# Optimization experiments

Measured on AMD Instinct MI355X. Metric: run time of the kernel, lower is better.

The kernel has to match this reference:

```python
import jax, jax.numpy as jnp
import numpy as np

B, C, H, W = 2, 128, 64, 64
D_STATE, D_CONV, EXPAND = 16, 4, 2
D_INNER = EXPAND * C
DT_RANK = (C + 15) // 16  # ceil(d_model/16) = 8


def layernorm(x, w, b):
    # WithBias_LayerNorm over last (channel) dim, unbiased=False variance
    mu = jnp.mean(x, axis=-1, keepdims=True)
    var = jnp.mean((x - mu) ** 2, axis=-1, keepdims=True)
    return (x - mu) / jnp.sqrt(var + 1e-5) * w + b


def causal_conv1d_silu(x, w, b):
    # x: (b, d, l); w: (d, k) depthwise; causal pad k-1 on left, then SiLU
    k = w.shape[1]
    out = jax.lax.conv_general_dilated(
        x, w[:, None, :], window_strides=(1,), padding=[(k - 1, 0)],
        dimension_numbers=('NCH', 'OIH', 'NCH'), feature_group_count=w.shape[0])
    return jax.nn.silu(out + b[:, None])


def selective_scan(dA, dBu, Cm):
    # dA, dBu: (b, d, l, n); Cm: (b, n, l) -> y: (b, d, l)
    dA_t = jnp.moveaxis(dA, 2, 0)    # (l, b, d, n)
    dBu_t = jnp.moveaxis(dBu, 2, 0)  # (l, b, d, n)
    C_t = jnp.moveaxis(Cm, 2, 0)     # (l, b, n)

    def step(h, inp):
        a, bu, c = inp
        h = a * h + bu
        y = jnp.einsum('bdn,bn->bd', h, c)
        return h, y

    h0 = jnp.zeros(dA.shape[:2] + (dA.shape[3],), dA.dtype)
    _, ys = jax.lax.scan(step, h0, (dA_t, dBu_t, C_t))
    return jnp.moveaxis(ys, 0, 2)  # (b, d, l)


def mamba_branch(x3, W_in, W_z, conv_w, conv_b, W_x, W_dt, b_dt, A, D, W_out):
    # x3: (b, l, d_model) normalized input
    x = jnp.einsum('bld,ed->bel', x3, W_in)  # (b, d_inner, l)
    z = jnp.einsum('bld,ed->bel', x3, W_z)
    x = causal_conv1d_silu(x, conv_w, conv_b)
    xdbl = jnp.einsum('bdl,ed->bel', x, W_x)  # (b, dt_rank+2n, l)
    dt_low = xdbl[:, :DT_RANK]
    Bm = xdbl[:, DT_RANK:DT_RANK + D_STATE]
    Cm = xdbl[:, DT_RANK + D_STATE:]
    delta = jax.nn.softplus(jnp.einsum('brl,dr->bdl', dt_low, W_dt) + b_dt[:, None])
    dA = jnp.exp(delta[:, :, :, None] * A[None, :, None, :])           # (b,d,l,n)
    dBu = jnp.einsum('bdl,bnl->bdln', delta * x, Bm)                    # (b,d,l,n)
    y = selective_scan(dA, dBu, Cm)
    y = y + D[:, None] * x
    y = y * jax.nn.silu(z)
    return jnp.einsum('bdl,od->blo', y, W_out)  # (b, l, d_model)


def setup_inputs() -> dict:
    key = jax.random.key(0)
    ks = jax.random.split(key, 24)
    rn = lambda k, shp, s: jax.random.normal(k, shp, dtype=jnp.float32) * s
    inp = {}
    inp['pan'] = rn(ks[0], (B, C, H, W), 1.0)
    inp['ms'] = rn(ks[1], (B, C, H, W), 1.0)
    inp['norm_w_pan'] = jnp.ones((C,), jnp.float32)
    inp['norm_b_pan'] = jnp.zeros((C,), jnp.float32)
    inp['norm_w_ms'] = jnp.ones((C,), jnp.float32)
    inp['norm_b_ms'] = jnp.zeros((C,), jnp.float32)
    inp['W_in_pan'] = rn(ks[2], (D_INNER, C), C ** -0.5)
    inp['W_in_ms'] = rn(ks[3], (D_INNER, C), C ** -0.5)
    inp['W_z_pan'] = rn(ks[4], (D_INNER, C), C ** -0.5)
    inp['W_z_ms'] = rn(ks[5], (D_INNER, C), C ** -0.5)
    inp['conv_w_pan'] = rn(ks[6], (D_INNER, D_CONV), D_CONV ** -0.5)
    inp['conv_b_pan'] = rn(ks[7], (D_INNER,), 0.02)
    inp['conv_w_ms'] = rn(ks[8], (D_INNER, D_CONV), D_CONV ** -0.5)
    inp['conv_b_ms'] = rn(ks[9], (D_INNER,), 0.02)
    inp['W_x_pan'] = rn(ks[10], (DT_RANK + 2 * D_STATE, D_INNER), D_INNER ** -0.5)
    inp['W_x_ms'] = rn(ks[11], (DT_RANK + 2 * D_STATE, D_INNER), D_INNER ** -0.5)
    dt_std = DT_RANK ** -0.5
    inp['W_dt_pan'] = jax.random.uniform(ks[12], (D_INNER, DT_RANK), jnp.float32, -dt_std, dt_std)
    inp['W_dt_ms'] = jax.random.uniform(ks[13], (D_INNER, DT_RANK), jnp.float32, -dt_std, dt_std)
    # dt bias init: inverse-softplus of dt ~ logU[1e-3, 1e-1]
    u = np.asarray(jax.random.uniform(ks[14], (D_INNER,)))
    dt = np.exp(u * (np.log(0.1) - np.log(0.001)) + np.log(0.001)).clip(min=1e-4)
    inv_dt = dt + np.log(-np.expm1(-dt))
    inp['b_dt_pan'] = jnp.asarray(inv_dt, jnp.float32)
    inp['b_dt_ms'] = jnp.asarray(inv_dt, jnp.float32)
    inp['A_log'] = jnp.log(jnp.broadcast_to(jnp.arange(1, D_STATE + 1, dtype=jnp.float32), (D_INNER, D_STATE)))
    inp['D_pan'] = jnp.ones((D_INNER,), jnp.float32)
    inp['D_ms'] = jnp.ones((D_INNER,), jnp.float32)
    inp['W_out_pan'] = rn(ks[15], (C, D_INNER), D_INNER ** -0.5)
    inp['W_out_ms'] = rn(ks[16], (C, D_INNER), D_INNER ** -0.5)
    return inp


def reference(pan, ms, norm_w_pan, norm_b_pan, norm_w_ms, norm_b_ms,
              W_in_pan, W_in_ms, W_z_pan, W_z_ms,
              conv_w_pan, conv_b_pan, conv_w_ms, conv_b_ms,
              W_x_pan, W_x_ms, W_dt_pan, W_dt_ms, b_dt_pan, b_dt_ms,
              A_log, D_pan, D_ms, W_out_pan, W_out_ms):
    b, c, h, w = pan.shape
    A = -jnp.exp(A_log)
    pan3 = layernorm(pan.reshape(b, c, h * w).transpose(0, 2, 1), norm_w_pan, norm_b_pan)
    ms3 = layernorm(ms.reshape(b, c, h * w).transpose(0, 2, 1), norm_w_ms, norm_b_ms)
    out_pan = mamba_branch(pan3, W_in_pan, W_z_pan, conv_w_pan, conv_b_pan,
                           W_x_pan, W_dt_pan, b_dt_pan, A, D_pan, W_out_pan)
    out_ms = mamba_branch(ms3, W_in_ms, W_z_ms, conv_w_ms, conv_b_ms,
                          W_x_ms, W_dt_ms, b_dt_ms, A, D_ms, W_out_ms)
    out_pan = out_pan.transpose(0, 2, 1).reshape(b, c, h, w)
    out_ms = out_ms.transpose(0, 2, 1).reshape(b, c, h, w)
    return (out_pan, out_ms)
```

## Files before the change

### kernel.cpp

```cpp
#include <hip/hip_runtime.h>
#include <hip/hip_bf16.h>

constexpr int BB = 2;
constexpr int CC = 128;
constexpr int LL = 4096;
constexpr int DI = 256;
constexpr int DS = 16;
constexpr int DR = 8;
constexpr int DX = 40;
constexpr int NZ = 2 * BB;
constexpr int CH = 8;
constexpr int NCH = LL / CH;
constexpr int SEG = 32;

typedef short bf16x8 __attribute__((ext_vector_type(8)));
typedef float f32x4 __attribute__((ext_vector_type(4)));

__device__ __forceinline__ unsigned short f2bf(float x) {
    __hip_bfloat16 h = __float2bfloat16(x);
    return *(unsigned short*)&h;
}
__device__ __forceinline__ float bflo(unsigned u) { return __uint_as_float(u << 16); }
__device__ __forceinline__ float bfhi(unsigned u) { return __uint_as_float(u & 0xffff0000u); }
__device__ __forceinline__ float bfu(unsigned short u) { return __uint_as_float((unsigned)u << 16); }
__device__ __forceinline__ float fast_rcp(float x) { return __builtin_amdgcn_rcpf(x); }
__device__ __forceinline__ float siluf(float x) { return x * fast_rcp(1.f + __expf(-x)); }
__device__ __forceinline__ float softplusf(float x) {
    const float z = exp2f(x * 1.44269504f);
    return (x > 20.f) ? x : 0.69314718f * log2f(1.f + z);
}

__global__ __launch_bounds__(256) void prep_kernel(
    const float* __restrict__ pan, const float* __restrict__ ms,
    const float* __restrict__ wpan, const float* __restrict__ bpan,
    const float* __restrict__ wms, const float* __restrict__ bms,
    const float* __restrict__ Winp, const float* __restrict__ Winm,
    const float* __restrict__ Wzp, const float* __restrict__ Wzm,
    const float* __restrict__ Woutp, const float* __restrict__ Woutm,
    const float* __restrict__ Wxp, const float* __restrict__ Wxm,
    unsigned short* __restrict__ x3b, unsigned short* __restrict__ wb)
{
    const int bx = blockIdx.x;
    const int t = threadIdx.x;
    if (bx >= 256) {
        const int i = (bx - 256) * 256 + t;
        const float* src; int off;
        if (i < 32768)       { src = Winp;  off = i; }
        else if (i < 65536)  { src = Winm;  off = i - 32768; }
        else if (i < 98304)  { src = Wzp;   off = i - 65536; }
        else if (i < 131072) { src = Wzm;   off = i - 98304; }
        else if (i < 163840) { src = Woutp; off = i - 131072; }
        else if (i < 196608) { src = Woutm; off = i - 163840; }
        else if (i < 206848) { src = Wxp;   off = i - 196608; }
        else                 { src = Wxm;   off = i - 206848; }
        wb[i] = f2bf(src[off]);
        return;
    }
    const int zi = bx >> 6;
    const int br = zi >> 1, b = zi & 1;
    const float* inp = br ? ms : pan;
    const float* wp = br ? wms : wpan;
    const float* bp = br ? bms : bpan;
    const int l0 = (bx & 63) * 64;
    const int lo = t & 63, c4 = t >> 6;
    const float* base = inp + (size_t)b * CC * LL + l0 + lo;
    float vals[32];
    float s = 0.f, s2 = 0.f;
    #pragma unroll
    for (int i = 0; i < 32; i++) {
        const int c = c4 * 32 + i;
        const float v = base[(size_t)c * LL];
        vals[i] = v; s += v; s2 += v * v;
    }
    __shared__ float red[2][4][64];
    red[0][c4][lo] = s; red[1][c4][lo] = s2;
    __syncthreads();
    const float S  = red[0][0][lo] + red[0][1][lo] + red[0][2][lo] + red[0][3][lo];
    const float S2 = red[1][0][lo] + red[1][1][lo] + red[1][2][lo] + red[1][3][lo];
    const float mu = S * (1.f / CC);
    const float var = S2 * (1.f / CC) - mu * mu;
    const float rstd = rsqrtf(var + 1e-5f);
    unsigned short* out = x3b + (size_t)zi * CC * LL + l0 + lo;
    #pragma unroll
    for (int i = 0; i < 32; i++) {
        const int c = c4 * 32 + i;
        out[(size_t)c * LL] = f2bf((vals[i] - mu) * rstd * wp[c] + bp[c]);
    }
}

__global__ __launch_bounds__(256) void gemm_inz_mfma(
    const unsigned short* __restrict__ wb, const unsigned short* __restrict__ x3b,
    unsigned short* __restrict__ xpre16, unsigned short* __restrict__ zb16)
{
    const int zi = blockIdx.z;
    const int my = blockIdx.y;
    const unsigned short* W = wb + (my >= 4 ? 65536 : 0) + (zi >= BB ? 32768 : 0);
    const int mbase = (my & 3) * 64;
    const unsigned short* Xb = x3b + (size_t)zi * CC * LL;
    const int n0 = blockIdx.x * 64;
    const int t = threadIdx.x;
    const int w = t >> 6, ln = t & 63;
    const int nf = ln & 15, qb = ln >> 4;
    bf16x8 afrag[4];
    const int mrow = mbase + w * 16 + nf;
    #pragma unroll
    for (int c = 0; c < 4; c++)
        afrag[c] = *(const bf16x8*)(W + (size_t)mrow * CC + c * 32 + qb * 8);
    __shared__ unsigned short Bs[64][40];
    unsigned* Bw = (unsigned*)Bs;
    f32x4 acc[4] = {};
    const int kp = t >> 4, n4 = (t & 15) * 4;
    #pragma unroll
    for (int kc = 0; kc < 4; kc++) {
        const ushort4 a0 = *(const ushort4*)(Xb + (size_t)(kc * 32 + 2 * kp) * LL + n0 + n4);
        const ushort4 a1 = *(const ushort4*)(Xb + (size_t)(kc * 32 + 2 * kp + 1) * LL + n0 + n4);
        if (kc) __syncthreads();
        Bw[(n4 + 0) * 20 + kp] = (unsigned)a0.x | ((unsigned)a1.x << 16);
        Bw[(n4 + 1) * 20 + kp] = (unsigned)a0.y | ((unsigned)a1.y << 16);
        Bw[(n4 + 2) * 20 + kp] = (unsigned)a0.z | ((unsigned)a1.z << 16);
        Bw[(n4 + 3) * 20 + kp] = (unsigned)a0.w | ((unsigned)a1.w << 16);
        __syncthreads();
        #pragma unroll
        for (int ns = 0; ns < 4; ns++) {
            const bf16x8 bf = *(const bf16x8*)(&Bs[ns * 16 + nf][qb * 8]);
            acc[ns] = __builtin_amdgcn_mfma_f32_16x16x32_bf16(afrag[kc], bf, acc[ns], 0, 0, 0);
        }
    }
    unsigned short* dst = (my >= 4) ? zb16 : xpre16;
    #pragma unroll
    for (int ns = 0; ns < 4; ns++)
        #pragma unroll
        for (int r = 0; r < 4; r++) {
            const int m = mbase + w * 16 + qb * 4 + r;
            dst[((size_t)zi * DI + m) * LL + n0 + ns * 16 + nf] = f2bf(acc[ns][r]);
        }
}

__global__ __launch_bounds__(256) void gemm_x_mfma(
    const unsigned short* __restrict__ wb, const unsigned short* __restrict__ xpre16,
    const float* __restrict__ cw0, const float* __restrict__ cb0,
    const float* __restrict__ cw1, const float* __restrict__ cb1,
    unsigned short* __restrict__ xc, unsigned short* __restrict__ xdbl16)
{
    const int zi = blockIdx.z;
    const unsigned short* W = wb + 196608 + (zi >= BB ? 10240 : 0);
    const float* cw = (zi >= BB) ? cw1 : cw0;
    const float* cb = (zi >= BB) ? cb1 : cb0;
    const unsigned short* Xb = xpre16 + (size_t)zi * DI * LL;
    unsigned short* xcb = xc + (size_t)zi * DI * LL;
    const int n0 = blockIdx.x * 64;
    const int t = threadIdx.x;
    const int w = t >> 6, ln = t & 63;
    const int nf = ln & 15, qb = ln >> 4;
    bf16x8 zfrag;
    #pragma unroll
    for (int j = 0; j < 8; j++) zfrag[j] = 0;
    bf16x8 afrag[8];
    const int mrow = w * 16 + nf;
    #pragma unroll
    for (int c = 0; c < 8; c++)
        afrag[c] = (mrow < DX) ? *(const bf16x8*)(W + (size_t)mrow * DI + c * 32 + qb * 8) : zfrag;
    __shared__ unsigned short Bs[64][40];
    unsigned* Bw = (unsigned*)Bs;
    f32x4 acc[4] = {};
    const int kp = t >> 4, n4 = (t & 15) * 4;
    #pragma unroll
    for (int kc = 0; kc < 8; kc++) {
        ushort4 o[2];
        #pragma unroll
        for (int rr = 0; rr < 2; rr++) {
            const int e = kc * 32 + 2 * kp + rr;
            const unsigned short* xp = Xb + (size_t)e * LL + n0 + n4;
            const ushort4 cur = *(const ushort4*)xp;
            float xm1, xm2, xm3;
            if (n0 + n4 == 0) { xm1 = 0.f; xm2 = 0.f; xm3 = 0.f; }
            else {
                const ushort4 prev = *(const ushort4*)(xp - 4);
                xm3 = bfu(prev.y); xm2 = bfu(prev.z); xm1 = bfu(prev.w);
            }
            const float c0 = bfu(cur.x), c1 = bfu(cur.y);
            const float c2 = bfu(cur.z), c3 = bfu(cur.w);
            const float w0 = cw[e * 4 + 0], w1 = cw[e * 4 + 1];
            const float w2 = cw[e * 4 + 2], w3 = cw[e * 4 + 3];
            const float bias = cb[e];
            o[rr].x = f2bf(siluf(w0 * xm3 + w1 * xm2 + w2 * xm1 + w3 * c0 + bias));
            o[rr].y = f2bf(siluf(w0 * xm2 + w1 * xm1 + w2 * c0 + w3 * c1 + bias));
            o[rr].z = f2bf(siluf(w0 * xm1 + w1 * c0 + w2 * c1 + w3 * c2 + bias));
            o[rr].w = f2bf(siluf(w0 * c0 + w1 * c1 + w2 * c2 + w3 * c3 + bias));
        }
        *(ushort4*)(xcb + (size_t)(kc * 32 + 2 * kp) * LL + n0 + n4) = o[0];
        *(ushort4*)(xcb + (size_t)(kc * 32 + 2 * kp + 1) * LL + n0 + n4) = o[1];
        if (kc) __syncthreads();
        Bw[(n4 + 0) * 20 + kp] = (unsigned)(unsigned short)o[0].x | ((unsigned)(unsigned short)o[1].x << 16);
        Bw[(n4 + 1) * 20 + kp] = (unsigned)(unsigned short)o[0].y | ((unsigned)(unsigned short)o[1].y << 16);
        Bw[(n4 + 2) * 20 + kp] = (unsigned)(unsigned short)o[0].z | ((unsigned)(unsigned short)o[1].z << 16);
        Bw[(n4 + 3) * 20 + kp] = (unsigned)(unsigned short)o[0].w | ((unsigned)(unsigned short)o[1].w << 16);
        __syncthreads();
        #pragma unroll
        for (int ns = 0; ns < 4; ns++) {
            const bf16x8 bf = *(const bf16x8*)(&Bs[ns * 16 + nf][qb * 8]);
            acc[ns] = __builtin_amdgcn_mfma_f32_16x16x32_bf16(afrag[kc], bf, acc[ns], 0, 0, 0);
        }
    }
    #pragma unroll
    for (int ns = 0; ns < 4; ns++)
        #pragma unroll
        for (int r = 0; r < 4; r++) {
            const int m = w * 16 + qb * 4 + r;
            if (m < DX)
                xdbl16[((size_t)zi * DX + m) * LL + n0 + ns * 16 + nf] = f2bf(acc[ns][r]);
        }
}

__global__ __launch_bounds__(256) void gemm_out_mfma(
    const unsigned short* __restrict__ wb, const unsigned short* __restrict__ yb,
    float* __restrict__ outg)
{
    const int zi = blockIdx.z;
    const unsigned short* W = wb + 131072 + (zi >= BB ? 32768 : 0);
    const int mbase = blockIdx.y * 64;
    const unsigned short* Xb = yb + (size_t)zi * DI * LL;
    const int n0 = blockIdx.x * 64;
    const int t = threadIdx.x;
    const int w = t >> 6, ln = t & 63;
    const int nf = ln & 15, qb = ln >> 4;
    bf16x8 afrag[8];
    const int mrow = mbase + w * 16 + nf;
    #pragma unroll
    for (int c = 0; c < 8; c++)
        afrag[c] = *(const bf16x8*)(W + (size_t)mrow * DI + c * 32 + qb * 8);
    __shared__ unsigned short Bs[64][40];
    unsigned* Bw = (unsigned*)Bs;
    f32x4 acc[4] = {};
    const int kp = t >> 4, n4 = (t & 15) * 4;
    #pragma unroll
    for (int kc = 0; kc < 8; kc++) {
        const ushort4 a0 = *(const ushort4*)(Xb + (size_t)(kc * 32 + 2 * kp) * LL + n0 + n4);
        const ushort4 a1 = *(const ushort4*)(Xb + (size_t)(kc * 32 + 2 * kp + 1) * LL + n0 + n4);
        if (kc) __syncthreads();
        Bw[(n4 + 0) * 20 + kp] = (unsigned)a0.x | ((unsigned)a1.x << 16);
        Bw[(n4 + 1) * 20 + kp] = (unsigned)a0.y | ((unsigned)a1.y << 16);
        Bw[(n4 + 2) * 20 + kp] = (unsigned)a0.z | ((unsigned)a1.z << 16);
        Bw[(n4 + 3) * 20 + kp] = (unsigned)a0.w | ((unsigned)a1.w << 16);
        __syncthreads();
        #pragma unroll
        for (int ns = 0; ns < 4; ns++) {
            const bf16x8 bf = *(const bf16x8*)(&Bs[ns * 16 + nf][qb * 8]);
            acc[ns] = __builtin_amdgcn_mfma_f32_16x16x32_bf16(afrag[kc], bf, acc[ns], 0, 0, 0);
        }
    }
    #pragma unroll
    for (int ns = 0; ns < 4; ns++)
        #pragma unroll
        for (int r = 0; r < 4; r++) {
            const int m = mbase + w * 16 + qb * 4 + r;
            outg[((size_t)zi * CC + m) * LL + n0 + ns * 16 + nf] = acc[ns][r];
        }
}

__global__ __launch_bounds__(512, 8) void scan_fused(
    const unsigned short* __restrict__ xc, const unsigned short* __restrict__ xdbl16,
    const float* __restrict__ A_log,
    const float* __restrict__ Wdt0, const float* __restrict__ Wdt1,
    const float* __restrict__ bdt0, const float* __restrict__ bdt1,
    const float* __restrict__ D0, const float* __restrict__ D1,
    const unsigned short* __restrict__ zb16, unsigned short* __restrict__ yb)
{
    const int blk = blockIdx.x;
    const int zi = blk >> 8;
    const int d  = blk & (DI - 1);
    const int t = threadIdx.x;
    const int l0 = t * CH;
    __shared__ float Ssh[DS * (NCH + 1)];
    __shared__ float sdl_sh[NCH];
    __shared__ float Pseg[DS * (SEG + 1)];
    __shared__ float Sseg[DS * (SEG + 1)];
    const unsigned short* xdb = xdbl16 + (size_t)zi * DX * LL;
    const float* Wdt = (zi >= BB) ? Wdt1 : Wdt0;
    const float* bdt = (zi >= BB) ? bdt1 : bdt0;
    const float dbias = bdt[d];
    float rx[CH];
    {
        const uint4 xv4 = *(const uint4*)(xc + (size_t)blk * LL + l0);
        rx[0] = bflo(xv4.x); rx[1] = bfhi(xv4.x);
        rx[2] = bflo(xv4.y); rx[3] = bfhi(xv4.y);
        rx[4] = bflo(xv4.z); rx[5] = bfhi(xv4.z);
        rx[6] = bflo(xv4.w); rx[7] = bfhi(xv4.w);
    }
    float e[CH], rdlx[CH];
    {
        float acc[CH];
        #pragma unroll
        for (int i = 0; i < CH; i++) acc[i] = dbias;
        #pragma unroll
        for (int r = 0; r < DR; r++) {
            const float wr = Wdt[d * DR + r];
            const uint4 v = *(const uint4*)(xdb + (size_t)r * LL + l0);
            acc[0] = fmaf(wr, bflo(v.x), acc[0]); acc[1] = fmaf(wr, bfhi(v.x), acc[1]);
            acc[2] = fmaf(wr, bflo(v.y), acc[2]); acc[3] = fmaf(wr, bfhi(v.y), acc[3]);
            acc[4] = fmaf(wr, bflo(v.z), acc[4]); acc[5] = fmaf(wr, bfhi(v.z), acc[5]);
            acc[6] = fmaf(wr, bflo(v.w), acc[6]); acc[7] = fmaf(wr, bfhi(v.w), acc[7]);
        }
        float sdl = 0.f;
        #pragma unroll
        for (int i = 0; i < CH; i++) {
            const float sp = softplusf(acc[i]);
            sdl += sp;
            rdlx[i] = sp * rx[i];
            e[i] = __expf(-sp);
        }
        sdl_sh[t] = sdl;
    }
    bool fast = true;
    #pragma unroll
    for (int n = 0; n < DS; n++)
        fast = fast && (fabsf(__expf(A_log[d * DS + n]) - (float)(n + 1)) < 1e-3f);
    const unsigned short* Bbase = xdb + (size_t)DR * LL;
    const unsigned short* Cbase = Bbase + (size_t)DS * LL;
    float y[CH];
    const int n2 = t & 15, sg = t >> 4;

    if (fast) {
        float pw[CH];
        #pragma unroll
        for (int i = 0; i < CH; i++) pw[i] = 1.f;
        #pragma unroll 4
        for (int n = 0; n < DS; n++) {
            const uint4 bv = *(const uint4*)(Bbase + (size_t)n * LL + l0);
            float hn = 0.f;
            pw[0] *= e[0]; hn = fmaf(pw[0], hn, rdlx[0] * bflo(bv.x));
            pw[1] *= e[1]; hn = fmaf(pw[1], hn, rdlx[1] * bfhi(bv.x));
            pw[2] *= e[2]; hn = fmaf(pw[2], hn, rdlx[2] * bflo(bv.y));
            pw[3] *= e[3]; hn = fmaf(pw[3], hn, rdlx[3] * bfhi(bv.y));
            pw[4] *= e[4]; hn = fmaf(pw[4], hn, rdlx[4] * bflo(bv.z));
            pw[5] *= e[5]; hn = fmaf(pw[5], hn, rdlx[5] * bfhi(bv.z));
            pw[6] *= e[6]; hn = fmaf(pw[6], hn, rdlx[6] * bflo(bv.w));
            pw[7] *= e[7]; hn = fmaf(pw[7], hn, rdlx[7] * bfhi(bv.w));
            Ssh[n * (NCH + 1) + t] = hn;
        }
        __syncthreads();
        {
            const float Ann = -(float)(n2 + 1);
            float P = 1.f, S = 0.f;
            #pragma unroll
            for (int k = 0; k < 16; k++) {
                const int c = sg * 16 + k;
                const float p = __expf(Ann * sdl_sh[c]);
                const float s = Ssh[n2 * (NCH + 1) + c];
                S = fmaf(p, S, s);
                P *= p;
            }
            Pseg[n2 * (SEG + 1) + sg] = P;
            Sseg[n2 * (SEG + 1) + sg] = S;
        }
        __syncthreads();
        if (t < DS) {
            float h = 0.f;
            #pragma unroll 4
            for (int c2 = 0; c2 < SEG; c2++) {
                const float p = Pseg[t * (SEG + 1) + c2];
                const float s = Sseg[t * (SEG + 1) + c2];
                Sseg[t * (SEG + 1) + c2] = h;
                h = fmaf(p, h, s);
            }
        }
        __syncthreads();
        {
            const float Ann = -(float)(n2 + 1);
            float h = Sseg[n2 * (SEG + 1) + sg];
            #pragma unroll
            for (int k = 0; k < 16; k++) {
                const int c = sg * 16 + k;
                const float p = __expf(Ann * sdl_sh[c]);
                const float s = Ssh[n2 * (NCH + 1) + c];
                Ssh[n2 * (NCH + 1) + c] = h;
                h = fmaf(p, h, s);
            }
        }
        __syncthreads();
        #pragma unroll
        for (int i = 0; i < CH; i++) { y[i] = 0.f; pw[i] = 1.f; }
        #pragma unroll 2
        for (int n = 0; n < DS; n++) {
            const uint4 bv = *(const uint4*)(Bbase + (size_t)n * LL + l0);
            const uint4 cv = *(const uint4*)(Cbase + (size_t)n * LL + l0);
            float hn = Ssh[n * (NCH + 1) + t];
            pw[0] *= e[0]; hn = fmaf(pw[0], hn, rdlx[0] * bflo(bv.x)); y[0] = fmaf(hn, bflo(cv.x), y[0]);
            pw[1] *= e[1]; hn = fmaf(pw[1], hn, rdlx[1] * bfhi(bv.x)); y[1] = fmaf(hn, bfhi(cv.x), y[1]);
            pw[2] *= e[2]; hn = fmaf(pw[2], hn, rdlx[2] * bflo(bv.y)); y[2] = fmaf(hn, bflo(cv.y), y[2]);
            pw[3] *= e[3]; hn = fmaf(pw[3], hn, rdlx[3] * bfhi(bv.y)); y[3] = fmaf(hn, bfhi(cv.y), y[3]);
            pw[4] *= e[4]; hn = fmaf(pw[4], hn, rdlx[4] * bflo(bv.z)); y[4] = fmaf(hn, bflo(cv.z), y[4]);
            pw[5] *= e[5]; hn = fmaf(pw[5], hn, rdlx[5] * bfhi(bv.z)); y[5] = fmaf(hn, bfhi(cv.z), y[5]);
            pw[6] *= e[6]; hn = fmaf(pw[6], hn, rdlx[6] * bflo(bv.w)); y[6] = fmaf(hn, bflo(cv.w), y[6]);
            pw[7] *= e[7]; hn = fmaf(pw[7], hn, rdlx[7] * bfhi(bv.w)); y[7] = fmaf(hn, bfhi(cv.w), y[7]);
        }
    } else {
        float rdl[CH];
        #pragma unroll
        for (int i = 0; i < CH; i++) rdl[i] = -0.69314718f * log2f(e[i]);
        #pragma unroll 2
        for (int n = 0; n < DS; n++) {
            const float An = -__expf(A_log[d * DS + n]);
            const uint4 bv = *(const uint4*)(Bbase + (size_t)n * LL + l0);
            float hn = 0.f;
            hn = fmaf(__expf(rdl[0] * An), hn, rdlx[0] * bflo(bv.x));
            hn = fmaf(__expf(rdl[1] * An), hn, rdlx[1] * bfhi(bv.x));
            hn = fmaf(__expf(rdl[2] * An), hn, rdlx[2] * bflo(bv.y));
            hn = fmaf(__expf(rdl[3] * An), hn, rdlx[3] * bfhi(bv.y));
            hn = fmaf(__expf(rdl[4] * An), hn, rdlx[4] * bflo(bv.z));
            hn = fmaf(__expf(rdl[5] * An), hn, rdlx[5] * bfhi(bv.z));
            hn = fmaf(__expf(rdl[6] * An), hn, rdlx[6] * bflo(bv.w));
            hn = fmaf(__expf(rdl[7] * An), hn, rdlx[7] * bfhi(bv.w));
            Ssh[n * (NCH + 1) + t] = hn;
        }
        __syncthreads();
        {
            const float Ann = -__expf(A_log[d * DS + n2]);
            float P = 1.f, S = 0.f;
            #pragma unroll
            for (int k = 0; k < 16; k++) {
                const int c = sg * 16 + k;
                const float p = __expf(Ann * sdl_sh[c]);
                const float s = Ssh[n2 * (NCH + 1) + c];
                S = fmaf(p, S, s);
                P *= p;
            }
            Pseg[n2 * (SEG + 1) + sg] = P;
            Sseg[n2 * (SEG + 1) + sg] = S;
        }
        __syncthreads();
        if (t < DS) {
            float h = 0.f;
            #pragma unroll 4
            for (int c2 = 0; c2 < SEG; c2++) {
                const float p = Pseg[t * (SEG + 1) + c2];
                const float s = Sseg[t * (SEG + 1) + c2];
                Sseg[t * (SEG + 1) + c2] = h;
                h = fmaf(p, h, s);
            }
        }
        __syncthreads();
        {
            const float Ann = -__expf(A_log[d * DS + n2]);
            float h = Sseg[n2 * (SEG + 1) + sg];
            #pragma unroll
            for (int k = 0; k < 16; k++) {
                const int c = sg * 16 + k;
                const float p = __expf(Ann * sdl_sh[c]);
                const float s = Ssh[n2 * (NCH + 1) + c];
                Ssh[n2 * (NCH + 1) + c] = h;
                h = fmaf(p, h, s);
            }
        }
        __syncthreads();
        #pragma unroll
        for (int i = 0; i < CH; i++) y[i] = 0.f;
        #pragma unroll 2
        for (int n = 0; n < DS; n++) {
            const float An = -__expf(A_log[d * DS + n]);
            const uint4 bv = *(const uint4*)(Bbase + (size_t)n * LL + l0);
            const uint4 cv = *(const uint4*)(Cbase + (size_t)n * LL + l0);
            float hn = Ssh[n * (NCH + 1) + t];
            hn = fmaf(__expf(rdl[0] * An), hn, rdlx[0] * bflo(bv.x)); y[0] = fmaf(hn, bflo(cv.x), y[0]);
            hn = fmaf(__expf(rdl[1] * An), hn, rdlx[1] * bfhi(bv.x)); y[1] = fmaf(hn, bfhi(cv.x), y[1]);
            hn = fmaf(__expf(rdl[2] * An), hn, rdlx[2] * bflo(bv.y)); y[2] = fmaf(hn, bflo(cv.y), y[2]);
            hn = fmaf(__expf(rdl[3] * An), hn, rdlx[3] * bfhi(bv.y)); y[3] = fmaf(hn, bfhi(cv.y), y[3]);
            hn = fmaf(__expf(rdl[4] * An), hn, rdlx[4] * bflo(bv.z)); y[4] = fmaf(hn, bflo(cv.z), y[4]);
            hn = fmaf(__expf(rdl[5] * An), hn, rdlx[5] * bfhi(bv.z)); y[5] = fmaf(hn, bfhi(cv.z), y[5]);
            hn = fmaf(__expf(rdl[6] * An), hn, rdlx[6] * bflo(bv.w)); y[6] = fmaf(hn, bflo(cv.w), y[6]);
            hn = fmaf(__expf(rdl[7] * An), hn, rdlx[7] * bfhi(bv.w)); y[7] = fmaf(hn, bfhi(cv.w), y[7]);
        }
    }
    const float Dd = ((zi >= BB) ? D1 : D0)[d];
    const unsigned short* z_g = zb16 + (size_t)blk * LL + l0;
    unsigned short* y_g = yb + (size_t)blk * LL + l0;
    {
        const uint4 zv = *(const uint4*)z_g;
        float zf[CH];
        zf[0] = bflo(zv.x); zf[1] = bfhi(zv.x); zf[2] = bflo(zv.y); zf[3] = bfhi(zv.y);
        zf[4] = bflo(zv.z); zf[5] = bfhi(zv.z); zf[6] = bflo(zv.w); zf[7] = bfhi(zv.w);
        ushort4 r0, r1;
        #pragma unroll
        for (int i = 0; i < CH; i++) {
            const float val = (y[i] + Dd * rx[i]) * siluf(zf[i]);
            if (i < 4) ((unsigned short*)&r0)[i] = f2bf(val);
            else       ((unsigned short*)&r1)[i - 4] = f2bf(val);
        }
        *(ushort4*)(y_g + 0) = r0;
        *(ushort4*)(y_g + 4) = r1;
    }
}

extern "C" void kernel_launch(void* const* d_in, const int* in_sizes, int n_in,
                              void* d_out, int out_size, void* d_ws, size_t ws_size,
                              hipStream_t stream)
{
    (void)in_sizes; (void)n_in; (void)out_size; (void)ws_size;
    auto fp = [&](int i) { return (const float*)d_in[i]; };
    const float *pan = fp(0), *ms = fp(1);
    const float *nwp = fp(2), *nbp = fp(3), *nwm = fp(4), *nbm = fp(5);
    const float *Winp = fp(6), *Winm = fp(7), *Wzp = fp(8), *Wzm = fp(9);
    const float *cwp = fp(10), *cbp = fp(11), *cwm = fp(12), *cbm = fp(13);
    const float *Wxp = fp(14), *Wxm = fp(15);
    const float *Wdtp = fp(16), *Wdtm = fp(17), *bdtp = fp(18), *bdtm = fp(19);
    const float *Alog = fp(20), *Dp = fp(21), *Dm = fp(22);
    const float *Woutp = fp(23), *Woutm = fp(24);

    unsigned short* us = (unsigned short*)d_ws;
    unsigned short* x3b    = us;
    unsigned short* xpre16 = x3b    + (size_t)NZ * CC * LL;
    unsigned short* zb16   = xpre16 + (size_t)NZ * DI * LL;
    unsigned short* xdbl16 = zb16   + (size_t)NZ * DI * LL;
    unsigned short* yb     = xdbl16 + (size_t)NZ * DX * LL;
    unsigned short* xc     = yb     + (size_t)NZ * DI * LL;
    unsigned short* wb     = xc     + (size_t)NZ * DI * LL;
    float* out = (float*)d_out;

    prep_kernel<<<dim3(256 + 848), 256, 0, stream>>>(
        pan, ms, nwp, nbp, nwm, nbm,
        Winp, Winm, Wzp, Wzm, Woutp, Woutm, Wxp, Wxm, x3b, wb);
    gemm_inz_mfma<<<dim3(LL / 64, 8, NZ), 256, 0, stream>>>(wb, x3b, xpre16, zb16);
    gemm_x_mfma<<<dim3(LL / 64, 1, NZ), 256, 0, stream>>>(wb, xpre16, cwp, cbp, cwm, cbm, xc, xdbl16);
    scan_fused<<<dim3(NZ * DI), 512, 0, stream>>>(xc, xdbl16, Alog, Wdtp, Wdtm, bdtp, bdtm,
                                                  Dp, Dm, zb16, yb);
    gemm_out_mfma<<<dim3(LL / 64, 2, NZ), 256, 0, stream>>>(wb, yb, out);
}
```

Before: 170.6 us.

## Share B tile between in/z GEMMs, prefetch next K-chunk, pack scan math into float2

The in/z projection kernel now computes both W_in and W_z outputs from one staged activation tile, which halves the grid and the activation reads. All three MFMA GEMM kernels load the next K-chunk from global memory into registers while the current chunk's MFMAs run. The scan kernel's dt projection and chunk recurrences are rewritten with float2 vectors so the compiler can emit packed FP32 operations. The costs are more live registers (two accumulator sets, prefetch buffers) and half as many blocks for the in/z GEMM.

```diff
diff --git a/kernel.cpp b/kernel.cpp
--- a/kernel.cpp
+++ b/kernel.cpp
@@ -15,6 +15,7 @@
 
 typedef short bf16x8 __attribute__((ext_vector_type(8)));
 typedef float f32x4 __attribute__((ext_vector_type(4)));
+typedef float f32x2 __attribute__((ext_vector_type(2)));
 
 __device__ __forceinline__ unsigned short f2bf(float x) {
     __hip_bfloat16 h = __float2bfloat16(x);
@@ -94,45 +95,53 @@
 {
     const int zi = blockIdx.z;
     const int my = blockIdx.y;
-    const unsigned short* W = wb + (my >= 4 ? 65536 : 0) + (zi >= BB ? 32768 : 0);
-    const int mbase = (my & 3) * 64;
+    const unsigned short* WI = wb + (zi >= BB ? 32768 : 0);
+    const unsigned short* WZ = WI + 65536;
+    const int mbase = my * 64;
     const unsigned short* Xb = x3b + (size_t)zi * CC * LL;
     const int n0 = blockIdx.x * 64;
     const int t = threadIdx.x;
     const int w = t >> 6, ln = t & 63;
     const int nf = ln & 15, qb = ln >> 4;
-    bf16x8 afrag[4];
+    bf16x8 afragI[4], afragZ[4];
     const int mrow = mbase + w * 16 + nf;
     #pragma unroll
-    for (int c = 0; c < 4; c++)
-        afrag[c] = *(const bf16x8*)(W + (size_t)mrow * CC + c * 32 + qb * 8);
+    for (int c = 0; c < 4; c++) {
+        afragI[c] = *(const bf16x8*)(WI + (size_t)mrow * CC + c * 32 + qb * 8);
+        afragZ[c] = *(const bf16x8*)(WZ + (size_t)mrow * CC + c * 32 + qb * 8);
+    }
     __shared__ unsigned short Bs[64][40];
     unsigned* Bw = (unsigned*)Bs;
-    f32x4 acc[4] = {};
+    f32x4 accI[4] = {}, accZ[4] = {};
     const int kp = t >> 4, n4 = (t & 15) * 4;
+    ushort4 a0 = *(const ushort4*)(Xb + (size_t)(2 * kp) * LL + n0 + n4);
+    ushort4 a1 = *(const ushort4*)(Xb + (size_t)(2 * kp + 1) * LL + n0 + n4);
     #pragma unroll
     for (int kc = 0; kc < 4; kc++) {
-        const ushort4 a0 = *(const ushort4*)(Xb + (size_t)(kc * 32 + 2 * kp) * LL + n0 + n4);
-        const ushort4 a1 = *(const ushort4*)(Xb + (size_t)(kc * 32 + 2 * kp + 1) * LL + n0 + n4);
         if (kc) __syncthreads();
         Bw[(n4 + 0) * 20 + kp] = (unsigned)a0.x | ((unsigned)a1.x << 16);
         Bw[(n4 + 1) * 20 + kp] = (unsigned)a0.y | ((unsigned)a1.y << 16);
         Bw[(n4 + 2) * 20 + kp] = (unsigned)a0.z | ((unsigned)a1.z << 16);
         Bw[(n4 + 3) * 20 + kp] = (unsigned)a0.w | ((unsigned)a1.w << 16);
         __syncthreads();
+        if (kc < 3) {
+            a0 = *(const ushort4*)(Xb + (size_t)((kc + 1) * 32 + 2 * kp) * LL + n0 + n4);
+            a1 = *(const ushort4*)(Xb + (size_t)((kc + 1) * 32 + 2 * kp + 1) * LL + n0 + n4);
+        }
         #pragma unroll
         for (int ns = 0; ns < 4; ns++) {
             const bf16x8 bf = *(const bf16x8*)(&Bs[ns * 16 + nf][qb * 8]);
-            acc[ns] = __builtin_amdgcn_mfma_f32_16x16x32_bf16(afrag[kc], bf, acc[ns], 0, 0, 0);
-        }
-    }
-    unsigned short* dst = (my >= 4) ? zb16 : xpre16;
+            accI[ns] = __builtin_amdgcn_mfma_f32_16x16x32_bf16(afragI[kc], bf, accI[ns], 0, 0, 0);
+            accZ[ns] = __builtin_amdgcn_mfma_f32_16x16x32_bf16(afragZ[kc], bf, accZ[ns], 0, 0, 0);
+        }
+    }
     #pragma unroll
     for (int ns = 0; ns < 4; ns++)
         #pragma unroll
         for (int r = 0; r < 4; r++) {
             const int m = mbase + w * 16 + qb * 4 + r;
-            dst[((size_t)zi * DI + m) * LL + n0 + ns * 16 + nf] = f2bf(acc[ns][r]);
+            xpre16[((size_t)zi * DI + m) * LL + n0 + ns * 16 + nf] = f2bf(accI[ns][r]);
+            zb16  [((size_t)zi * DI + m) * LL + n0 + ns * 16 + nf] = f2bf(accZ[ns][r]);
         }
 }
 
@@ -164,20 +173,24 @@
     unsigned* Bw = (unsigned*)Bs;
     f32x4 acc[4] = {};
     const int kp = t >> 4, n4 = (t & 15) * 4;
+    const bool edge = (n0 + n4 == 0);
+    ushort4 cur0, cur1, prv0, prv1;
+    {
+        const unsigned short* xp0 = Xb + (size_t)(2 * kp) * LL + n0 + n4;
+        const unsigned short* xp1 = Xb + (size_t)(2 * kp + 1) * LL + n0 + n4;
+        cur0 = *(const ushort4*)xp0; cur1 = *(const ushort4*)xp1;
+        if (!edge) { prv0 = *(const ushort4*)(xp0 - 4); prv1 = *(const ushort4*)(xp1 - 4); }
+        else { prv0 = ushort4{0,0,0,0}; prv1 = ushort4{0,0,0,0}; }
+    }
     #pragma unroll
     for (int kc = 0; kc < 8; kc++) {
         ushort4 o[2];
         #pragma unroll
         for (int rr = 0; rr < 2; rr++) {
             const int e = kc * 32 + 2 * kp + rr;
-            const unsigned short* xp = Xb + (size_t)e * LL + n0 + n4;
-            const ushort4 cur = *(const ushort4*)xp;
-            float xm1, xm2, xm3;
-            if (n0 + n4 == 0) { xm1 = 0.f; xm2 = 0.f; xm3 = 0.f; }
-            else {
-                const ushort4 prev = *(const ushort4*)(xp - 4);
-                xm3 = bfu(prev.y); xm2 = bfu(prev.z); xm1 = bfu(prev.w);
-            }
+            const ushort4 cur = rr ? cur1 : cur0;
+            const ushort4 prv = rr ? prv1 : prv0;
+            const float xm3 = bfu(prv.y), xm2 = bfu(prv.z), xm1 = bfu(prv.w);
             const float c0 = bfu(cur.x), c1 = bfu(cur.y);
             const float c2 = bfu(cur.z), c3 = bfu(cur.w);
             const float w0 = cw[e * 4 + 0], w1 = cw[e * 4 + 1];
@@ -196,6 +209,12 @@
         Bw[(n4 + 2) * 20 + kp] = (unsigned)(unsigned short)o[0].z | ((unsigned)(unsigned short)o[1].z << 16);
         Bw[(n4 + 3) * 20 + kp] = (unsigned)(unsigned short)o[0].w | ((unsigned)(unsigned short)o[1].w << 16);
         __syncthreads();
+        if (kc < 7) {
+            const unsigned short* xp0 = Xb + (size_t)((kc + 1) * 32 + 2 * kp) * LL + n0 + n4;
+            const unsigned short* xp1 = Xb + (size_t)((kc + 1) * 32 + 2 * kp + 1) * LL + n0 + n4;
+            cur0 = *(const ushort4*)xp0; cur1 = *(const ushort4*)xp1;
+            if (!edge) { prv0 = *(const ushort4*)(xp0 - 4); prv1 = *(const ushort4*)(xp1 - 4); }
+        }
         #pragma unroll
         for (int ns = 0; ns < 4; ns++) {
             const bf16x8 bf = *(const bf16x8*)(&Bs[ns * 16 + nf][qb * 8]);
@@ -233,16 +252,20 @@
     unsigned* Bw = (unsigned*)Bs;
     f32x4 acc[4] = {};
     const int kp = t >> 4, n4 = (t & 15) * 4;
+    ushort4 a0 = *(const ushort4*)(Xb + (size_t)(2 * kp) * LL + n0 + n4);
+    ushort4 a1 = *(const ushort4*)(Xb + (size_t)(2 * kp + 1) * LL + n0 + n4);
     #pragma unroll
     for (int kc = 0; kc < 8; kc++) {
-        const ushort4 a0 = *(const ushort4*)(Xb + (size_t)(kc * 32 + 2 * kp) * LL + n0 + n4);
-        const ushort4 a1 = *(const ushort4*)(Xb + (size_t)(kc * 32 + 2 * kp + 1) * LL + n0 + n4);
         if (kc) __syncthreads();
         Bw[(n4 + 0) * 20 + kp] = (unsigned)a0.x | ((unsigned)a1.x << 16);
         Bw[(n4 + 1) * 20 + kp] = (unsigned)a0.y | ((unsigned)a1.y << 16);
         Bw[(n4 + 2) * 20 + kp] = (unsigned)a0.z | ((unsigned)a1.z << 16);
         Bw[(n4 + 3) * 20 + kp] = (unsigned)a0.w | ((unsigned)a1.w << 16);
         __syncthreads();
+        if (kc < 7) {
+            a0 = *(const ushort4*)(Xb + (size_t)((kc + 1) * 32 + 2 * kp) * LL + n0 + n4);
+            a1 = *(const ushort4*)(Xb + (size_t)((kc + 1) * 32 + 2 * kp + 1) * LL + n0 + n4);
+        }
         #pragma unroll
         for (int ns = 0; ns < 4; ns++) {
             const bf16x8 bf = *(const bf16x8*)(&Bs[ns * 16 + nf][qb * 8]);
@@ -289,22 +312,26 @@
     }
     float e[CH], rdlx[CH];
     {
-        float acc[CH];
-        #pragma unroll
-        for (int i = 0; i < CH; i++) acc[i] = dbias;
+        f32x2 acc2[4];
+        #pragma unroll
+        for (int j = 0; j < 4; j++) acc2[j] = f32x2{dbias, dbias};
         #pragma unroll
         for (int r = 0; r < DR; r++) {
             const float wr = Wdt[d * DR + r];
+            const f32x2 w2 = {wr, wr};
             const uint4 v = *(const uint4*)(xdb + (size_t)r * LL + l0);
-            acc[0] = fmaf(wr, bflo(v.x), acc[0]); acc[1] = fmaf(wr, bfhi(v.x), acc[1]);
-            acc[2] = fmaf(wr, bflo(v.y), acc[2]); acc[3] = fmaf(wr, bfhi(v.y), acc[3]);
-            acc[4] = fmaf(wr, bflo(v.z), acc[4]); acc[5] = fmaf(wr, bfhi(v.z), acc[5]);
-            acc[6] = fmaf(wr, bflo(v.w), acc[6]); acc[7] = fmaf(wr, bfhi(v.w), acc[7]);
-        }
+            acc2[0] = w2 * f32x2{bflo(v.x), bfhi(v.x)} + acc2[0];
+            acc2[1] = w2 * f32x2{bflo(v.y), bfhi(v.y)} + acc2[1];
+            acc2[2] = w2 * f32x2{bflo(v.z), bfhi(v.z)} + acc2[2];
+            acc2[3] = w2 * f32x2{bflo(v.w), bfhi(v.w)} + acc2[3];
+        }
+        float av[CH];
+        av[0] = acc2[0].x; av[1] = acc2[0].y; av[2] = acc2[1].x; av[3] = acc2[1].y;
+        av[4] = acc2[2].x; av[5] = acc2[2].y; av[6] = acc2[3].x; av[7] = acc2[3].y;
         float sdl = 0.f;
         #pragma unroll
         for (int i = 0; i < CH; i++) {
-            const float sp = softplusf(acc[i]);
+            const float sp = softplusf(av[i]);
             sdl += sp;
             rdlx[i] = sp * rx[i];
             e[i] = __expf(-sp);
@@ -321,21 +348,33 @@
     const int n2 = t & 15, sg = t >> 4;
 
     if (fast) {
-        float pw[CH];
-        #pragma unroll
-        for (int i = 0; i < CH; i++) pw[i] = 1.f;
+        f32x2 e2[4], rdlx2[4];
+        #pragma unroll
+        for (int j = 0; j < 4; j++) {
+            e2[j] = f32x2{e[2 * j], e[2 * j + 1]};
+            rdlx2[j] = f32x2{rdlx[2 * j], rdlx[2 * j + 1]};
+        }
+        f32x2 pw2[4];
+        #pragma unroll
+        for (int j = 0; j < 4; j++) pw2[j] = f32x2{1.f, 1.f};
         #pragma unroll 4
         for (int n = 0; n < DS; n++) {
             const uint4 bv = *(const uint4*)(Bbase + (size_t)n * LL + l0);
-            float hn = 0.f;
-            pw[0] *= e[0]; hn = fmaf(pw[0], hn, rdlx[0] * bflo(bv.x));
-            pw[1] *= e[1]; hn = fmaf(pw[1], hn, rdlx[1] * bfhi(bv.x));
-            pw[2] *= e[2]; hn = fmaf(pw[2], hn, rdlx[2] * bflo(bv.y));
-            pw[3] *= e[3]; hn = fmaf(pw[3], hn, rdlx[3] * bfhi(bv.y));
-            pw[4] *= e[4]; hn = fmaf(pw[4], hn, rdlx[4] * bflo(bv.z));
-            pw[5] *= e[5]; hn = fmaf(pw[5], hn, rdlx[5] * bfhi(bv.z));
-            pw[6] *= e[6]; hn = fmaf(pw[6], hn, rdlx[6] * bflo(bv.w));
-            pw[7] *= e[7]; hn = fmaf(pw[7], hn, rdlx[7] * bfhi(bv.w));
+            const f32x2 b0 = {bflo(bv.x), bfhi(bv.x)};
+            const f32x2 b1 = {bflo(bv.y), bfhi(bv.y)};
+            const f32x2 b2 = {bflo(bv.z), bfhi(bv.z)};
+            const f32x2 b3 = {bflo(bv.w), bfhi(bv.w)};
+            pw2[0] *= e2[0]; pw2[1] *= e2[1]; pw2[2] *= e2[2]; pw2[3] *= e2[3];
+            const f32x2 u0 = rdlx2[0] * b0, u1 = rdlx2[1] * b1;
+            const f32x2 u2 = rdlx2[2] * b2, u3 = rdlx2[3] * b3;
+            float hn = u0.x;
+            hn = fmaf(pw2[0].y, hn, u0.y);
+            hn = fmaf(pw2[1].x, hn, u1.x);
+            hn = fmaf(pw2[1].y, hn, u1.y);
+            hn = fmaf(pw2[2].x, hn, u2.x);
+            hn = fmaf(pw2[2].y, hn, u2.y);
+            hn = fmaf(pw2[3].x, hn, u3.x);
+            hn = fmaf(pw2[3].y, hn, u3.y);
             Ssh[n * (NCH + 1) + t] = hn;
         }
         __syncthreads();
@@ -378,22 +417,40 @@
             }
         }
         __syncthreads();
-        #pragma unroll
-        for (int i = 0; i < CH; i++) { y[i] = 0.f; pw[i] = 1.f; }
+        f32x2 y2[4];
+        #pragma unroll
+        for (int j = 0; j < 4; j++) { y2[j] = f32x2{0.f, 0.f}; pw2[j] = f32x2{1.f, 1.f}; }
         #pragma unroll 2
         for (int n = 0; n < DS; n++) {
             const uint4 bv = *(const uint4*)(Bbase + (size_t)n * LL + l0);
             const uint4 cv = *(const uint4*)(Cbase + (size_t)n * LL + l0);
-            float hn = Ssh[n * (NCH + 1) + t];
-            pw[0] *= e[0]; hn = fmaf(pw[0], hn, rdlx[0] * bflo(bv.x)); y[0] = fmaf(hn, bflo(cv.x), y[0]);
-            pw[1] *= e[1]; hn = fmaf(pw[1], hn, rdlx[1] * bfhi(bv.x)); y[1] = fmaf(hn, bfhi(cv.x), y[1]);
-            pw[2] *= e[2]; hn = fmaf(pw[2], hn, rdlx[2] * bflo(bv.y)); y[2] = fmaf(hn, bflo(cv.y), y[2]);
-            pw[3] *= e[3]; hn = fmaf(pw[3], hn, rdlx[3] * bfhi(bv.y)); y[3] = fmaf(hn, bfhi(cv.y), y[3]);
-            pw[4] *= e[4]; hn = fmaf(pw[4], hn, rdlx[4] * bflo(bv.z)); y[4] = fmaf(hn, bflo(cv.z), y[4]);
-            pw[5] *= e[5]; hn = fmaf(pw[5], hn, rdlx[5] * bfhi(bv.z)); y[5] = fmaf(hn, bfhi(cv.z), y[5]);
-            pw[6] *= e[6]; hn = fmaf(pw[6], hn, rdlx[6] * bflo(bv.w)); y[6] = fmaf(hn, bflo(cv.w), y[6]);
-            pw[7] *= e[7]; hn = fmaf(pw[7], hn, rdlx[7] * bfhi(bv.w)); y[7] = fmaf(hn, bfhi(cv.w), y[7]);
-        }
+            const f32x2 b0 = {bflo(bv.x), bfhi(bv.x)};
+            const f32x2 b1 = {bflo(bv.y), bfhi(bv.y)};
+            const f32x2 b2 = {bflo(bv.z), bfhi(bv.z)};
+            const f32x2 b3 = {bflo(bv.w), bfhi(bv.w)};
+            const f32x2 c0 = {bflo(cv.x), bfhi(cv.x)};
+            const f32x2 c1 = {bflo(cv.y), bfhi(cv.y)};
+            const f32x2 c2 = {bflo(cv.z), bfhi(cv.z)};
+            const f32x2 c3 = {bflo(cv.w), bfhi(cv.w)};
+            pw2[0] *= e2[0]; pw2[1] *= e2[1]; pw2[2] *= e2[2]; pw2[3] *= e2[3];
+            const f32x2 u0 = rdlx2[0] * b0, u1 = rdlx2[1] * b1;
+            const f32x2 u2 = rdlx2[2] * b2, u3 = rdlx2[3] * b3;
+            const float hp = Ssh[n * (NCH + 1) + t];
+            const float h0 = fmaf(pw2[0].x, hp, u0.x);
+            const float h1 = fmaf(pw2[0].y, h0, u0.y);
+            y2[0] = f32x2{h0, h1} * c0 + y2[0];
+            const float h2 = fmaf(pw2[1].x, h1, u1.x);
+            const float h3 = fmaf(pw2[1].y, h2, u1.y);
+            y2[1] = f32x2{h2, h3} * c1 + y2[1];
+            const float h4 = fmaf(pw2[2].x, h3, u2.x);
+            const float h5 = fmaf(pw2[2].y, h4, u2.y);
+            y2[2] = f32x2{h4, h5} * c2 + y2[2];
+            const float h6 = fmaf(pw2[3].x, h5, u3.x);
+            const float h7 = fmaf(pw2[3].y, h6, u3.y);
+            y2[3] = f32x2{h6, h7} * c3 + y2[3];
+        }
+        y[0] = y2[0].x; y[1] = y2[0].y; y[2] = y2[1].x; y[3] = y2[1].y;
+        y[4] = y2[2].x; y[5] = y2[2].y; y[6] = y2[3].x; y[7] = y2[3].y;
     } else {
         float rdl[CH];
         #pragma unroll
@@ -519,7 +576,7 @@
     prep_kernel<<<dim3(256 + 848), 256, 0, stream>>>(
         pan, ms, nwp, nbp, nwm, nbm,
         Winp, Winm, Wzp, Wzm, Woutp, Woutm, Wxp, Wxm, x3b, wb);
-    gemm_inz_mfma<<<dim3(LL / 64, 8, NZ), 256, 0, stream>>>(wb, x3b, xpre16, zb16);
+    gemm_inz_mfma<<<dim3(LL / 64, 4, NZ), 256, 0, stream>>>(wb, x3b, xpre16, zb16);
     gemm_x_mfma<<<dim3(LL / 64, 1, NZ), 256, 0, stream>>>(wb, xpre16, cwp, cbp, cwm, cbm, xc, xdbl16);
     scan_fused<<<dim3(NZ * DI), 512, 0, stream>>>(xc, xdbl16, Alog, Wdtp, Wdtm, bdtp, bdtm,
                                                   Dp, Dm, zb16, yb);
```

Result: no change. 167.8 us (-1.7%).
